# Kernel optimization log

Hardware: AMD Instinct MI355X
Metric: run time of the kernel (lower is better)

## Reference

```python
import jax, jax.numpy as jnp
import numpy as np

NY, NX = 800, 700  # BEV grid from voxel_feature_shape[2], voxel_feature_shape[3]
NCH = 2            # voxel_feature_shape[1] + 1 = occupancy + intensity


def setup_inputs() -> dict:
    key = jax.random.key(0)
    N, T, B = 200000, 32, 16
    k1, k2, k3, k4, k5 = jax.random.split(key, 5)
    vox_feats = jax.random.normal(k1, (N, T, 5), dtype=jnp.float32)
    num_points = jax.random.randint(k2, (N,), 1, T + 1, dtype=jnp.int32)
    b = jax.random.randint(k3, (N, 1), 0, B, dtype=jnp.int32)
    y = jax.random.randint(k4, (N, 1), 0, NY, dtype=jnp.int32)
    x = jax.random.randint(k5, (N, 1), 0, NX, dtype=jnp.int32)
    z = jnp.zeros((N, 1), dtype=jnp.int32)
    coords = jnp.concatenate([b, z, y, x], axis=1)  # [N, 4] = (batch, z, y, x)
    return {"vox_feats": vox_feats, "num_points": num_points,
            "coords": coords, "batch_size": B}


def reference(vox_feats, num_points, coords, batch_size):
    # intensity: mean over points per voxel, last feature channel -> [N]
    intensity = vox_feats.mean(axis=1)[:, -1]
    # occupancy value is 1.0 for every non-empty voxel (ones_like(num_points))
    # fuse the per-batch loop into one global scatter with batch-offset indices
    flat = (coords[:, 0].astype(jnp.int32) * (NY * NX)
            + coords[:, 2].astype(jnp.int32) * NX
            + coords[:, 3].astype(jnp.int32))  # [N]
    occ = jnp.zeros((batch_size * NY * NX,), dtype=vox_feats.dtype).at[flat].set(1.0)
    inten = jnp.zeros((batch_size * NY * NX,), dtype=vox_feats.dtype).at[flat].set(intensity)
    # [B, 2, NY, NX]
    return jnp.stack([occ.reshape(batch_size, NY, NX),
                      inten.reshape(batch_size, NY, NX)], axis=1)
```

## Files before the change

kernel.cpp:

```cpp
#include <hip/hip_runtime.h>
#include <hip/hip_bf16.h>


#define PX_NY 800
#define PX_NX 700
#define PX_T  32
#define PX_C  5
#define ROW_F4 (PX_T * PX_C / 4)

__global__ void __launch_bounds__(256)
pixor_k1(const float4* __restrict__ vox4,
         const int4*   __restrict__ coords4,
         float*        __restrict__ intens,
         unsigned int* __restrict__ vote,
         float4*       __restrict__ out4,
         int N, int P, int zq) {
    const int tid = blockIdx.x * 256 + threadIdx.x;
    const int nth = gridDim.x * 256;

    const float4 z = make_float4(0.f, 0.f, 0.f, 0.f);
    for (int i = tid; i < zq; i += nth) out4[i] = z;

    for (int n = tid; n < N; n += nth) {
        const float4* rp = vox4 + (size_t)n * ROW_F4;
        float s = 0.f;
#pragma unroll
        for (int g = 0; g < 8; ++g) {
            float4 a = rp[g * 5 + 1];
            float4 b = rp[g * 5 + 2];
            float4 c = rp[g * 5 + 3];
            float4 d = rp[g * 5 + 4];
            s += (a.x + b.y) + (c.z + d.w);
        }
        intens[n] = s * (1.0f / (float)PX_T);

        int4 c4 = coords4[n];
        unsigned cell = (unsigned)(c4.x * P + c4.z * PX_NX + c4.w);
        unsigned key  = (unsigned)(n + 1);

        unsigned old = atomicCAS(vote + cell, 0u, key);
        if (old != 0u) {
            while (true) {
                bool valid = (old - 1u) < (unsigned)N;
                if (valid && old >= key) break;
                unsigned prev = atomicCAS(vote + cell, old, key);
                if (prev == old) break;
                old = prev;
            }
        }
    }
}

__global__ void __launch_bounds__(256)
pixor_k2(const int4*   __restrict__ coords4,
         const float*  __restrict__ intens,
         unsigned int* __restrict__ vote,
         float*        __restrict__ out,
         int N, int P) {
    int n = blockIdx.x * 256 + threadIdx.x;
    if (n >= N) return;

    int4 c4 = coords4[n];
    int yx = c4.z * PX_NX + c4.w;
    unsigned cell = (unsigned)(c4.x * P + yx);

    unsigned v = atomicAdd(vote + cell, 0u);
    if (v == (unsigned)(n + 1)) {
        int base = c4.x * (2 * P) + yx;
        out[base]     = 1.0f;
        out[base + P] = intens[n];
    }
}

extern "C" void kernel_launch(void* const* d_in, const int* in_sizes, int n_in,
                              void* d_out, int out_size, void* d_ws, size_t ws_size,
                              hipStream_t stream) {
    const float* vox    = (const float*)d_in[0];
    const int*   coords = (const int*)d_in[2];
    float* out = (float*)d_out;

    const int N  = in_sizes[1];
    const int P  = PX_NY * PX_NX;
    const int B  = out_size / (2 * P);
    const int zq = out_size / 4;

    unsigned int* ws_vote = (unsigned int*)d_ws;
    float*        ws_int  = (float*)d_ws + (size_t)B * P;

    const int BLK = 256;

    pixor_k1<<<2048, BLK, 0, stream>>>((const float4*)vox, (const int4*)coords,
                                       ws_int, ws_vote, (float4*)out,
                                       N, P, zq);

    pixor_k2<<<(N + BLK - 1) / BLK, BLK, 0, stream>>>((const int4*)coords,
                                                      ws_int, ws_vote, out,
                                                      N, P);
}
```

Before: 52.01 us.

## Stage voxel tiles through LDS with coalesced loads for intensity reduction

Instead of each thread reading its own 640-byte voxel row with strided float4 loads, each block now loads a 64-voxel tile with fully coalesced float4 loads. It scatters only the intensity channel into padded shared memory, then reduces each row with 4 lanes and warp shuffles. The intent is better memory coalescing for the dominant input read. In exchange it adds two block barriers per tile, and only one lane in four now does the voting atomics.

```diff
diff --git a/kernel.cpp b/kernel.cpp
--- a/kernel.cpp
+++ b/kernel.cpp
@@ -6,7 +6,10 @@
 #define PX_NX 700
 #define PX_T  32
 #define PX_C  5
-#define ROW_F4 (PX_T * PX_C / 4)
+#define ROW_F4 40
+#define TILE   64
+#define TILE_F4 (TILE * ROW_F4)
+#define LPAD   33
 
 __global__ void __launch_bounds__(256)
 pixor_k1(const float4* __restrict__ vox4,
@@ -15,39 +18,67 @@
          unsigned int* __restrict__ vote,
          float4*       __restrict__ out4,
          int N, int P, int zq) {
-    const int tid = blockIdx.x * 256 + threadIdx.x;
-    const int nth = gridDim.x * 256;
+    __shared__ float lsl[TILE * LPAD];
+
+    const int tid  = threadIdx.x;
+    const int gtid = blockIdx.x * 256 + tid;
+    const int nth  = gridDim.x * 256;
 
     const float4 z = make_float4(0.f, 0.f, 0.f, 0.f);
-    for (int i = tid; i < zq; i += nth) out4[i] = z;
+    for (int i = gtid; i < zq; i += nth) out4[i] = z;
 
-    for (int n = tid; n < N; n += nth) {
-        const float4* rp = vox4 + (size_t)n * ROW_F4;
+    const int ntiles = (N + TILE - 1) / TILE;
+    const int totF4  = N * ROW_F4;
+
+    for (int t = blockIdx.x; t < ntiles; t += gridDim.x) {
+        const int base = t * TILE_F4;
+
+#pragma unroll
+        for (int k = 0; k < 10; ++k) {
+            int i  = k * 256 + tid;
+            int gi = base + i;
+            if (gi < totF4) {
+                float4 f = vox4[gi];
+                int row = i / ROW_F4;
+                int j   = i - row * ROW_F4;
+                int sub = j % 5;
+                if (sub) {
+                    float v = (sub == 1) ? f.x
+                            : (sub == 2) ? f.y
+                            : (sub == 3) ? f.z : f.w;
+                    int tp = (4 * j + (sub - 1) - 4) / 5;
+                    lsl[row * LPAD + tp] = v;
+                }
+            }
+        }
+        __syncthreads();
+
+        int row = tid >> 2, q = tid & 3;
+        const float* rp = &lsl[row * LPAD + q * 8];
         float s = 0.f;
 #pragma unroll
-        for (int g = 0; g < 8; ++g) {
-            float4 a = rp[g * 5 + 1];
-            float4 b = rp[g * 5 + 2];
-            float4 c = rp[g * 5 + 3];
-            float4 d = rp[g * 5 + 4];
-            s += (a.x + b.y) + (c.z + d.w);
-        }
-        intens[n] = s * (1.0f / (float)PX_T);
+        for (int m = 0; m < 8; ++m) s += rp[m];
+        s += __shfl_xor(s, 1);
+        s += __shfl_xor(s, 2);
 
-        int4 c4 = coords4[n];
-        unsigned cell = (unsigned)(c4.x * P + c4.z * PX_NX + c4.w);
-        unsigned key  = (unsigned)(n + 1);
+        int grow = t * TILE + row;
+        if (q == 0 && grow < N) {
+            float inten = s * (1.0f / (float)PX_T);
+            intens[grow] = inten;
 
-        unsigned old = atomicCAS(vote + cell, 0u, key);
-        if (old != 0u) {
-            while (true) {
-                bool valid = (old - 1u) < (unsigned)N;
-                if (valid && old >= key) break;
+            int4 c4 = coords4[grow];
+            unsigned cell = (unsigned)(c4.x * P + c4.z * PX_NX + c4.w);
+            unsigned key  = (unsigned)(grow + 1);
+
+            unsigned old = atomicCAS(vote + cell, 0u, key);
+            while (old != 0u) {
+                if ((old - 1u) < (unsigned)N && old >= key) break;
                 unsigned prev = atomicCAS(vote + cell, old, key);
                 if (prev == old) break;
                 old = prev;
             }
         }
+        __syncthreads();
     }
 }
 
```

Result: faster. 46.69 us (-10.2%).
